# Performance work log

Hardware: AMD Instinct MI355X
Metric: run time of the kernel (lower is better)

The kernel has to match this reference:

```python
import jax, jax.numpy as jnp
import numpy as np

I_SIZE = 4096
H_SIZE = 2048
WIN = 10          # window_size
MAX_DEPTH = 6
EPS = 1e-9


def setup_inputs() -> dict:
    key = jax.random.key(0)
    ks = jax.random.split(key, 10)
    u = lambda k, s: jax.random.uniform(k, s, dtype=jnp.float32)
    n = lambda k, s: jax.random.normal(k, s, dtype=jnp.float32) * 0.02
    return {
        "input": u(ks[0], (WIN, I_SIZE)),
        "stack": u(ks[1], (1, H_SIZE, I_SIZE)),
        "stack_pointer": u(ks[2], (1, H_SIZE)),
        "input_pointer": u(ks[3], (1, WIN + 1)),
        "ff_w": n(ks[4], (I_SIZE, I_SIZE)), "ff_b": jnp.zeros((I_SIZE,), jnp.float32),
        "gate_w": n(ks[5], (2, 1)), "gate_b": jnp.zeros((2,), jnp.float32),
        "kin_w": n(ks[6], (I_SIZE, 2 * I_SIZE)), "kin_b": jnp.zeros((I_SIZE,), jnp.float32),
        "kouth_w": n(ks[7], (I_SIZE, I_SIZE)), "kouth_b": jnp.zeros((I_SIZE,), jnp.float32),
        "kouti_w": n(ks[8], (I_SIZE, I_SIZE)), "kouti_b": jnp.zeros((I_SIZE,), jnp.float32),
    }


def _forward(input, stack, stack_pointer, input_pointer,
             ff_w, ff_b, gate_w, gate_b, kin_w, kin_b,
             kouth_w, kouth_b, kouti_w, kouti_b):
    lsm = jax.nn.log_softmax
    lin = lambda x, w, b: jnp.matmul(x, w.T) + b

    def push(vec, stk, ptr):
        # stk: [1,H,I], ptr: [1,H], vec: [1,I] or [1,1,I]
        stk = stk * (1.0 - ptr)[..., None] + jnp.matmul(ptr[..., None], vec)
        ptr_new = jnp.concatenate([jnp.zeros((ptr.shape[0], 1), ptr.dtype), ptr[:, :-1]], axis=-1)
        return stk, ptr_new

    def pop(stk, ptr):
        ptr_new = jnp.concatenate([ptr[:, 1:], jnp.zeros((ptr.shape[0], 1), ptr.dtype)], axis=-1)
        s = jnp.sum(ptr_new, -1)                      # [1]
        norm = jnp.where(s > 0, ptr_new / jnp.where(s > 0, s, 1.0), ptr_new)
        outvec = jnp.matmul(norm, stk)                # [1,1,I]
        stk_new = (1.0 - ptr_new)[..., None] * stk
        ptr_new = ptr_new.at[:, 0].add(ptr[:, 0])
        return outvec, stk_new, ptr_new

    def get(inp, ptr):
        outvec = jnp.matmul(ptr[:, :-1], inp)         # [1,I]
        ptr_new = jnp.concatenate([jnp.zeros((ptr.shape[0], 1), ptr.dtype), ptr[:, :-1]], axis=-1)
        ptr_new = ptr_new.at[:, -1].add(ptr[:, -1])
        return outvec, ptr_new

    def kld(p, q):
        p = p + EPS
        q = q + EPS
        p = p / jnp.sum(p)
        q = q / jnp.sum(q)
        return jnp.sum(p * jnp.log(p / q))

    def calforward(invec, hvec):
        predvec = lsm(lin(hvec, ff_w, ff_b))
        perp_pred = kld(predvec, invec)
        inp_cat = jnp.concatenate([invec.reshape(1, 1, -1), hvec.reshape(1, 1, -1)], axis=-1)
        new_inp = jnp.exp(lsm(lin(inp_cat, kin_w, kin_b)))      # softmax, [1,1,I]
        proj_hvec = jnp.exp(lsm(lin(new_inp, kouth_w, kouth_b)))
        proj_invec = jnp.exp(lsm(lin(new_inp, kouti_w, kouti_b)))
        perp = perp_pred + kld(proj_invec, invec) / 2 + kld(proj_hvec, hvec) / 2
        gate = jnp.exp(lsm(lin(perp_pred.reshape(1), gate_w, gate_b)))  # [2]
        gate = jnp.where(jnp.sum(hvec) == 0, jnp.array([1.0, 0.0], gate.dtype),
                         jnp.where(jnp.sum(invec) == 0, jnp.array([0.0, 1.0], gate.dtype), gate))
        return gate, perp, new_inp

    stackmem, sptrmem, iptrmem, wldl, perps = [], [], [], [], []
    for ii in range(MAX_DEPTH):
        if ii == 0:
            invec, st1, sp1 = pop(stack, stack_pointer)
            hvec, st1, sp1 = pop(st1, sp1)
            gate, perp, new_inp = calforward(invec, hvec)
            st1, sp1 = push(new_inp, st1, sp1)
            stackmem.append(st1); sptrmem.append(sp1); iptrmem.append(input_pointer)
            wldl.append(gate[1]); perps.append(perp)
        else:
            ip2, st2, sp2 = input_pointer, stack, stack_pointer
            for _ in range(ii - 1):
                invec, ip2 = get(input, ip2)
                st2, sp2 = push(invec, st2, sp2)
            invec, ip2 = get(input, ip2)
            hvec, st2, sp2 = pop(st2, sp2)
            gate, perp, new_inp = calforward(invec, hvec)
            st2, sp2 = push(new_inp, st2, sp2)
            stackmem.append(st2); sptrmem.append(sp2); iptrmem.append(ip2)
            input_avail = 1.0 - ip2[0, -1]
            wldl.append((1.0 - wldl[ii - 1]) * gate[1] * input_avail)
            perps.append(perp)

    w = jnp.stack(wldl)
    w = w / jnp.sum(w)
    resperp = jnp.sum(w * jnp.stack(perps))
    new_stack = sum(w[i] * stackmem[i] for i in range(MAX_DEPTH))
    new_sp = sum(w[i] * sptrmem[i] for i in range(MAX_DEPTH))
    new_ip = sum(w[i] * iptrmem[i] for i in range(MAX_DEPTH))
    ssum = jnp.sum(new_sp, -1, keepdims=True)
    new_sp = jnp.where(ssum > 0, new_sp / jnp.where(ssum > 0, ssum, 1.0), new_sp)
    isum = jnp.sum(new_ip, -1, keepdims=True)
    new_ip = jnp.where(isum > 0, new_ip / jnp.where(isum > 0, isum, 1.0), new_ip)
    return resperp, new_stack, new_sp, new_ip


def reference(input, stack, stack_pointer, input_pointer,
              ff_w, ff_b, gate_w, gate_b, kin_w, kin_b,
              kouth_w, kouth_b, kouti_w, kouti_b):
    return _forward(input, stack, stack_pointer, input_pointer,
                    ff_w, ff_b, gate_w, gate_b, kin_w, kin_b,
                    kouth_w, kouth_b, kouti_w, kouti_b)
```

## Files before the change

kernel.cpp:

```cpp
#include <hip/hip_runtime.h>
#include <cfloat>
#include <cmath>

#define HH   2048
#define ISZ  4096
#define WN   10
#define ND   6
#define EPSF 1e-9f

#define O_WROW   0
#define O_GETW   14336
#define O_POPC   14464
#define O_AVAIL  14496
#define O_SCAL   14528
#define O_IPTR   14592
#define O_DFIN   14720
#define O_CNEW   27008
#define O_CFIN   39296
#define O_SPTR   88448
#define O_MW     100736
#define O_CEFF   104832
#define O_R      125312
#define O_NEWINP 153984
#define O_G      178560
#define O_HVEC   199040
#define O_IVEC   223616
#define O_YFF    248192
#define O_Z      272768
#define O_YH     297344
#define O_YI     321920

__device__ __forceinline__ float blockReduceSum(float v, float* sm){
  int ln = threadIdx.x & 63, w = threadIdx.x >> 6;
  #pragma unroll
  for (int o=32;o>0;o>>=1) v += __shfl_down(v,o);
  if (ln==0) sm[w]=v;
  __syncthreads();
  if (threadIdx.x==0){
    float r=0.f; int nw=(int)(blockDim.x>>6);
    for (int i=0;i<nw;i++) r+=sm[i];
    sm[16]=r;
  }
  __syncthreads();
  float r = sm[16];
  __syncthreads();
  return r;
}

__device__ __forceinline__ float blockReduceMax(float v, float* sm){
  int ln = threadIdx.x & 63, w = threadIdx.x >> 6;
  #pragma unroll
  for (int o=32;o>0;o>>=1) v = fmaxf(v,__shfl_down(v,o));
  if (ln==0) sm[w]=v;
  __syncthreads();
  if (threadIdx.x==0){
    float r=-FLT_MAX; int nw=(int)(blockDim.x>>6);
    for (int i=0;i<nw;i++) r=fmaxf(r,sm[i]);
    sm[16]=r;
  }
  __syncthreads();
  float r = sm[16];
  __syncthreads();
  return r;
}

__global__ __launch_bounds__(1024) void k_ptr_prep(
    const float* __restrict__ sp0g, const float* __restrict__ ip0g,
    float* __restrict__ ws)
{
  __shared__ float sp[HH], q[HH], D[HH];
  __shared__ float c[4][HH];
  __shared__ float red[17];
  const int d   = blockIdx.x;
  const int tid = threadIdx.x;

  float* Wrow = ws + O_WROW;
  float* getW = ws + O_GETW;
  float* popc = ws + O_POPC;
  float* Dfin = ws + O_DFIN;
  float* cnew = ws + O_CNEW;
  float* cfin = ws + O_CFIN;
  float* sptr = ws + O_SPTR;
  float* iptr = ws + O_IPTR;
  float* avail= ws + O_AVAIL;

  if (d==0 && tid==0){
    float ip[WN+1], nip[WN+1];
    for (int k=0;k<=WN;k++) ip[k]=ip0g[k];
    for (int k=0;k<=WN;k++) iptr[k]=ip[k];
    avail[0] = 1.f - ip[WN];
    for (int t=0;t<5;t++){
      for (int k=0;k<WN;k++) getW[t*16+k]=ip[k];
      nip[0]=0.f;
      for (int k=1;k<=WN;k++) nip[k]=ip[k-1];
      nip[WN] += ip[WN];
      for (int k=0;k<=WN;k++) ip[k]=nip[k];
      for (int k=0;k<=WN;k++) iptr[(t+1)*16+k]=ip[k];
      avail[t+1] = 1.f - ip[WN];
    }
  }

  #pragma unroll
  for (int jj=0;jj<2;jj++){ int j=tid+jj*1024; sp[j]=sp0g[j]; D[j]=1.f; }
  __syncthreads();

  if (d==0){
    #pragma unroll
    for (int jj=0;jj<2;jj++){ int j=tid+jj*1024; q[j]=(j<HH-1)? sp[j+1]:0.f; }
    float ls=0.f;
    #pragma unroll
    for (int jj=0;jj<2;jj++) ls += q[tid+jj*1024];
    float s = blockReduceSum(ls, red);
    float sc = (s>0.f)? 1.f/s : 1.f;
    #pragma unroll
    for (int jj=0;jj<2;jj++){
      int j=tid+jj*1024;
      float qq=q[j];
      Wrow[j] = qq*sc;
      D[j] = 1.f - qq;
      sp[j] = qq + ((j==0)? sp[0] : 0.f);
    }
    __syncthreads();
    #pragma unroll
    for (int jj=0;jj<2;jj++){ int j=tid+jj*1024; q[j]=(j<HH-1)? sp[j+1]:0.f; }
    ls=0.f;
    #pragma unroll
    for (int jj=0;jj<2;jj++) ls += q[tid+jj*1024];
    s = blockReduceSum(ls, red);
    sc = (s>0.f)? 1.f/s : 1.f;
    #pragma unroll
    for (int jj=0;jj<2;jj++){
      int j=tid+jj*1024;
      float qq=q[j];
      Wrow[HH+j] = qq*sc*D[j];
      D[j] *= (1.f-qq);
      sp[j] = qq + ((j==0)? sp[0] : 0.f);
    }
    __syncthreads();
    #pragma unroll
    for (int jj=0;jj<2;jj++){
      int j=tid+jj*1024;
      float p=sp[j];
      Dfin[j] = D[j]*(1.f-p);
      cnew[j] = p;
      sptr[j] = (j==0)? 0.f : sp[j-1];
    }
  } else {
    const int nterms = d-1;
    for (int t=0;t<nterms;t++){
      #pragma unroll
      for (int jj=0;jj<2;jj++){
        int j=tid+jj*1024;
        float p=sp[j], f=1.f-p;
        D[j]*=f;
        for (int u=0;u<t;u++) c[u][j]*=f;
        c[t][j]=p;
      }
      __syncthreads();
      float sv[2];
      #pragma unroll
      for (int jj=0;jj<2;jj++){ int j=tid+jj*1024; sv[jj]=(j==0)?0.f:sp[j-1]; }
      __syncthreads();
      #pragma unroll
      for (int jj=0;jj<2;jj++){ int j=tid+jj*1024; sp[j]=sv[jj]; }
      __syncthreads();
    }
    #pragma unroll
    for (int jj=0;jj<2;jj++){ int j=tid+jj*1024; q[j]=(j<HH-1)? sp[j+1]:0.f; }
    float ls=0.f;
    #pragma unroll
    for (int jj=0;jj<2;jj++) ls += q[tid+jj*1024];
    float s = blockReduceSum(ls, red);
    float sc = (s>0.f)? 1.f/s : 1.f;
    for (int t=0;t<nterms;t++){
      float pc=0.f;
      #pragma unroll
      for (int jj=0;jj<2;jj++){ int j=tid+jj*1024; pc += q[j]*sc*c[t][j]; }
      pc = blockReduceSum(pc, red);
      if (tid==0) popc[d*4+t]=pc;
    }
    #pragma unroll
    for (int jj=0;jj<2;jj++){
      int j=tid+jj*1024;
      float qq=q[j];
      Wrow[(1+d)*HH+j] = qq*sc*D[j];
      float f = 1.f-qq;
      D[j] *= f;
      for (int t=0;t<nterms;t++) c[t][j] *= f;
      sp[j] = qq + ((j==0)? sp[0] : 0.f);
    }
    __syncthreads();
    #pragma unroll
    for (int jj=0;jj<2;jj++){
      int j=tid+jj*1024;
      float p=sp[j], f=1.f-p;
      Dfin[d*HH+j] = D[j]*f;
      for (int t=0;t<nterms;t++) cfin[(d*4+t)*HH+j] = c[t][j]*f;
      cnew[d*HH+j] = p;
      sptr[d*HH+j] = (j==0)? 0.f : sp[j-1];
    }
  }
}

__global__ __launch_bounds__(256) void k_rowsum(
    const float* __restrict__ stk, const float* __restrict__ wrow,
    float* __restrict__ R)
{
  __shared__ float wsh[7][64];
  const int col = blockIdx.x*256 + threadIdx.x;
  const int r0  = blockIdx.y*64;
  for (int idx=threadIdx.x; idx<7*64; idx+=256){
    int k=idx>>6, r=idx&63;
    wsh[k][r]=wrow[k*HH + r0 + r];
  }
  __syncthreads();
  float a0=0,a1=0,a2=0,a3=0,a4=0,a5=0,a6=0;
  const float* sp = stk + (size_t)r0*ISZ + col;
  #pragma unroll 4
  for (int r=0;r<64;r++){
    float v = sp[(size_t)r*ISZ];
    a0+=wsh[0][r]*v; a1+=wsh[1][r]*v; a2+=wsh[2][r]*v; a3+=wsh[3][r]*v;
    a4+=wsh[4][r]*v; a5+=wsh[5][r]*v; a6+=wsh[6][r]*v;
  }
  atomicAdd(&R[0*ISZ+col],a0); atomicAdd(&R[1*ISZ+col],a1);
  atomicAdd(&R[2*ISZ+col],a2); atomicAdd(&R[3*ISZ+col],a3);
  atomicAdd(&R[4*ISZ+col],a4); atomicAdd(&R[5*ISZ+col],a5);
  atomicAdd(&R[6*ISZ+col],a6);
}

__global__ void k_gvec(const float* __restrict__ input,
                       const float* __restrict__ getW, float* __restrict__ g)
{
  int idx = blockIdx.x*256+threadIdx.x;
  if (idx >= 5*ISZ) return;
  int t = idx / ISZ, cx = idx % ISZ;
  float acc=0.f;
  #pragma unroll
  for (int k=0;k<WN;k++) acc += getW[t*16+k]*input[k*ISZ + cx];
  g[idx] = acc;
}

__global__ void k_build_hv(const float* __restrict__ R, const float* __restrict__ g,
                           const float* __restrict__ popc,
                           float* __restrict__ Hvec, float* __restrict__ Ivec)
{
  int idx = blockIdx.x*256+threadIdx.x;
  if (idx >= ND*ISZ) return;
  int d = idx/ISZ, cx = idx%ISZ;
  if (d==0){ Ivec[idx]=R[cx]; Hvec[idx]=R[ISZ+cx]; }
  else {
    Ivec[idx]=g[(d-1)*ISZ+cx];
    float h = R[(1+d)*ISZ+cx];
    for (int t=0;t<=d-2;t++) h += popc[d*4+t]*g[t*ISZ+cx];
    Hvec[idx]=h;
  }
}

__global__ __launch_bounds__(1024) void k_matvec6(
    const float* __restrict__ W, int ldw,
    const float* __restrict__ X, const float* __restrict__ bias,
    float* __restrict__ Y, int nrows, int accumulate)
{
  __shared__ float xs[6*ISZ];
  for (int idx=threadIdx.x; idx<6*ISZ; idx+=1024) xs[idx]=X[idx];
  __syncthreads();
  const int wv = threadIdx.x>>6, ln = threadIdx.x&63;
  const int row = blockIdx.x*16 + wv;
  if (row < nrows){
    const float* wr = W + (size_t)row*ldw;
    float a[6]={0,0,0,0,0,0};
    #pragma unroll 4
    for (int k=ln*4; k<ISZ; k+=256){
      float4 w4 = *(const float4*)(wr + k);
      #pragma unroll
      for (int d=0; d<6; d++){
        float4 x4 = *(const float4*)(xs + d*ISZ + k);
        a[d] += w4.x*x4.x + w4.y*x4.y + w4.z*x4.z + w4.w*x4.w;
      }
    }
    #pragma unroll
    for (int d=0;d<6;d++){
      float v = a[d];
      #pragma unroll
      for (int o=32;o>0;o>>=1) v += __shfl_down(v,o);
      if (ln==0){
        float r = v + (bias? bias[row] : 0.f);
        if (accumulate) Y[d*ISZ+row] += r;
        else            Y[d*ISZ+row]  = r;
      }
    }
  }
}

__global__ __launch_bounds__(1024) void k_s1(
    const float* __restrict__ yff, const float* __restrict__ zz,
    const float* __restrict__ Ivec, const float* __restrict__ Hvec,
    const float* __restrict__ gate_w, const float* __restrict__ gate_b,
    float* __restrict__ newinp, float* __restrict__ scal)
{
  __shared__ float sm[17];
  const int d = blockIdx.x, tid = threadIdx.x;
  const float* y  = yff + d*ISZ;
  const float* z  = zz  + d*ISZ;
  const float* iv = Ivec + d*ISZ;
  const float* hv = Hvec + d*ISZ;

  float m=-FLT_MAX;
  for (int cx=tid;cx<ISZ;cx+=1024) m=fmaxf(m,y[cx]);
  m = blockReduceMax(m,sm);
  float se=0.f;
  for (int cx=tid;cx<ISZ;cx+=1024) se += expf(y[cx]-m);
  se = blockReduceSum(se,sm);
  float lse = m + logf(se);

  float sP=0.f,sQ=0.f,sI=0.f,sH=0.f;
  for (int cx=tid;cx<ISZ;cx+=1024){
    sP += (y[cx]-lse)+EPSF;
    float ivv=iv[cx];
    sQ += ivv+EPSF; sI += ivv; sH += hv[cx];
  }
  sP=blockReduceSum(sP,sm); sQ=blockReduceSum(sQ,sm);
  sI=blockReduceSum(sI,sm); sH=blockReduceSum(sH,sm);

  float kk=0.f;
  for (int cx=tid;cx<ISZ;cx+=1024){
    float ph = ((y[cx]-lse)+EPSF)/sP;
    float qh = (iv[cx]+EPSF)/sQ;
    kk += ph*(logf(ph)-logf(qh));
  }
  kk = blockReduceSum(kk,sm);

  float m2=-FLT_MAX;
  for (int cx=tid;cx<ISZ;cx+=1024) m2=fmaxf(m2,z[cx]);
  m2=blockReduceMax(m2,sm);
  float se2=0.f;
  for (int cx=tid;cx<ISZ;cx+=1024) se2 += expf(z[cx]-m2);
  se2=blockReduceSum(se2,sm);
  float inv2=1.f/se2;
  for (int cx=tid;cx<ISZ;cx+=1024) newinp[d*ISZ+cx] = expf(z[cx]-m2)*inv2;

  if (tid==0){
    float pp=kk;
    float a0=gate_w[0]*pp+gate_b[0];
    float a1=gate_w[1]*pp+gate_b[1];
    float mg=fmaxf(a0,a1);
    float e0=expf(a0-mg), e1=expf(a1-mg);
    float g1=e1/(e0+e1);
    if (sH==0.f) g1=0.f;
    else if (sI==0.f) g1=1.f;
    scal[d]=pp; scal[6+d]=g1;
  }
}

__device__ float kld_softmax_vs(const float* __restrict__ lg,
                                const float* __restrict__ qv, float* sm)
{
  const int tid=threadIdx.x;
  float m=-FLT_MAX;
  for (int cx=tid;cx<ISZ;cx+=1024) m=fmaxf(m,lg[cx]);
  m=blockReduceMax(m,sm);
  float se=0.f;
  for (int cx=tid;cx<ISZ;cx+=1024) se+=expf(lg[cx]-m);
  se=blockReduceSum(se,sm);
  float inv=1.f/se;
  float sp=0.f,sq=0.f;
  for (int cx=tid;cx<ISZ;cx+=1024){ sp += expf(lg[cx]-m)*inv + EPSF; sq += qv[cx]+EPSF; }
  sp=blockReduceSum(sp,sm); sq=blockReduceSum(sq,sm);
  float kk=0.f;
  for (int cx=tid;cx<ISZ;cx+=1024){
    float ph=(expf(lg[cx]-m)*inv+EPSF)/sp;
    float qh=(qv[cx]+EPSF)/sq;
    kk += ph*(logf(ph)-logf(qh));
  }
  return blockReduceSum(kk,sm);
}

__global__ __launch_bounds__(1024) void k_s2(
    const float* __restrict__ yh, const float* __restrict__ yi,
    const float* __restrict__ Ivec, const float* __restrict__ Hvec,
    float* __restrict__ scal)
{
  __shared__ float sm[17];
  const int d=blockIdx.x;
  float kh = kld_softmax_vs(yh+d*ISZ, Hvec+d*ISZ, sm);
  float ki = kld_softmax_vs(yi+d*ISZ, Ivec+d*ISZ, sm);
  if (threadIdx.x==0) scal[12+d] = scal[d] + ki*0.5f + kh*0.5f;
}

__global__ void k_s3(float* __restrict__ ws, float* __restrict__ out){
  if (threadIdx.x==0 && blockIdx.x==0){
    const float* gate1 = ws + O_SCAL + 6;
    const float* perp  = ws + O_SCAL + 12;
    const float* avail = ws + O_AVAIL;
    float wl[ND];
    wl[0] = gate1[0];
    for (int i=1;i<ND;i++) wl[i] = (1.f - wl[i-1]) * gate1[i] * avail[i];
    float s=0.f; for (int i=0;i<ND;i++) s += wl[i];
    float rp=0.f;
    for (int i=0;i<ND;i++){ float wn = wl[i]/s; ws[O_SCAL+18+i]=wn; rp += wn*perp[i]; }
    out[0]=rp;
  }
}

__global__ __launch_bounds__(1024) void k_combine(float* __restrict__ ws,
                                                  float* __restrict__ out){
  __shared__ float sm[17];
  const int tid = threadIdx.x;
  float w[ND];
  #pragma unroll
  for (int d=0;d<ND;d++) w[d] = ws[O_SCAL+18+d];
  const float* Dfin = ws+O_DFIN; const float* cnew = ws+O_CNEW;
  const float* cfin = ws+O_CFIN; const float* sptr = ws+O_SPTR;
  float snl[2]; float mysum=0.f;
  for (int jj=0;jj<2;jj++){
    int j = tid + jj*1024;
    float mw=0.f, sn=0.f;
    float ce[10];
    #pragma unroll
    for (int d=0;d<ND;d++){
      mw += w[d]*Dfin[d*HH+j];
      sn += w[d]*sptr[d*HH+j];
      ce[d] = w[d]*cnew[d*HH+j];
    }
    #pragma unroll
    for (int t=0;t<4;t++){
      float a=0.f;
      for (int d=t+2;d<ND;d++) a += w[d]*cfin[(d*4+t)*HH+j];
      ce[6+t]=a;
    }
    ws[O_MW+j]=mw;
    #pragma unroll
    for (int v=0;v<10;v++) ws[O_CEFF + j*10 + v] = ce[v];
    snl[jj]=sn; mysum+=sn;
  }
  float ssum = blockReduceSum(mysum, sm);
  for (int jj=0;jj<2;jj++){
    int j = tid + jj*1024;
    out[1 + (size_t)HH*ISZ + j] = (ssum>0.f)? snl[jj]/ssum : snl[jj];
  }
  if (tid==0){
    const float* iptr = ws+O_IPTR;
    float ipn[WN+1]; float is=0.f;
    for (int k=0;k<=WN;k++){
      float a=0.f;
      for (int d=0;d<ND;d++) a += w[d]*iptr[d*16+k];
      ipn[k]=a; is+=a;
    }
    size_t base = 1 + (size_t)HH*ISZ + HH;
    for (int k=0;k<=WN;k++) out[base+k] = (is>0.f)? ipn[k]/is : ipn[k];
  }
}

__global__ __launch_bounds__(256) void k_stack_out(
    const float* __restrict__ stk, const float* __restrict__ V,
    const float* __restrict__ Mw, const float* __restrict__ Ceff,
    float* __restrict__ out)
{
  __shared__ float Vt[10*1024];
  const int c0 = blockIdx.x*1024;
  const int j0 = blockIdx.y*8;
  for (int idx=threadIdx.x; idx<10*1024; idx+=256){
    int v=idx>>10, cc=idx&1023;
    Vt[idx] = V[v*ISZ + c0 + cc];
  }
  __syncthreads();
  const int tx4 = threadIdx.x*4;
  for (int r=0;r<8;r++){
    int j=j0+r;
    float mw = Mw[j];
    float ce[10];
    #pragma unroll
    for (int v=0;v<10;v++) ce[v]=Ceff[j*10+v];
    float4 sv = *(const float4*)(stk + (size_t)j*ISZ + c0 + tx4);
    float o0 = mw*sv.x, o1 = mw*sv.y, o2 = mw*sv.z, o3 = mw*sv.w;
    #pragma unroll
    for (int v=0;v<10;v++){
      const float* vr = Vt + v*1024 + tx4;
      float cv=ce[v];
      o0 += cv*vr[0]; o1 += cv*vr[1]; o2 += cv*vr[2]; o3 += cv*vr[3];
    }
    float* op = out + 1 + (size_t)j*ISZ + c0 + tx4;
    op[0]=o0; op[1]=o1; op[2]=o2; op[3]=o3;
  }
}

extern "C" void kernel_launch(void* const* d_in, const int* in_sizes, int n_in,
                              void* d_out, int out_size, void* d_ws, size_t ws_size,
                              hipStream_t stream)
{
  (void)in_sizes; (void)n_in; (void)out_size; (void)ws_size;
  const float* input   = (const float*)d_in[0];
  const float* stack   = (const float*)d_in[1];
  const float* sp0     = (const float*)d_in[2];
  const float* ip0     = (const float*)d_in[3];
  const float* ff_w    = (const float*)d_in[4];
  const float* ff_b    = (const float*)d_in[5];
  const float* gate_w  = (const float*)d_in[6];
  const float* gate_b  = (const float*)d_in[7];
  const float* kin_w   = (const float*)d_in[8];
  const float* kin_b   = (const float*)d_in[9];
  const float* kouth_w = (const float*)d_in[10];
  const float* kouth_b = (const float*)d_in[11];
  const float* kouti_w = (const float*)d_in[12];
  const float* kouti_b = (const float*)d_in[13];
  float* out = (float*)d_out;
  float* ws  = (float*)d_ws;

  k_ptr_prep<<<ND,1024,0,stream>>>(sp0, ip0, ws);
  hipMemsetAsync(ws + O_R, 0, (size_t)7*ISZ*sizeof(float), stream);
  k_rowsum<<<dim3(16,32),256,0,stream>>>(stack, ws+O_WROW, ws+O_R);
  k_gvec<<<(5*ISZ+255)/256,256,0,stream>>>(input, ws+O_GETW, ws+O_G);
  k_build_hv<<<(ND*ISZ+255)/256,256,0,stream>>>(ws+O_R, ws+O_G, ws+O_POPC,
                                                ws+O_HVEC, ws+O_IVEC);
  k_matvec6<<<256,1024,0,stream>>>(kin_w,      8192, ws+O_IVEC, kin_b,   ws+O_Z,   ISZ, 0);
  k_matvec6<<<256,1024,0,stream>>>(ff_w,       4096, ws+O_HVEC, ff_b,    ws+O_YFF, ISZ, 0);
  k_matvec6<<<256,1024,0,stream>>>(kin_w+4096, 8192, ws+O_HVEC, nullptr, ws+O_Z,   ISZ, 1);
  k_s1<<<ND,1024,0,stream>>>(ws+O_YFF, ws+O_Z, ws+O_IVEC, ws+O_HVEC,
                             gate_w, gate_b, ws+O_NEWINP, ws+O_SCAL);
  k_matvec6<<<256,1024,0,stream>>>(kouth_w, 4096, ws+O_NEWINP, kouth_b, ws+O_YH, ISZ, 0);
  k_matvec6<<<256,1024,0,stream>>>(kouti_w, 4096, ws+O_NEWINP, kouti_b, ws+O_YI, ISZ, 0);
  k_s2<<<ND,1024,0,stream>>>(ws+O_YH, ws+O_YI, ws+O_IVEC, ws+O_HVEC, ws+O_SCAL);
  k_s3<<<1,64,0,stream>>>(ws, out);
  k_combine<<<1,1024,0,stream>>>(ws, out);
  k_stack_out<<<dim3(4,256),256,0,stream>>>(stack, ws+O_NEWINP, ws+O_MW, ws+O_CEFF, out);
}
```

Before: 209.5 us.

## Merge launches: batch matvecs, fuse vector build, single-pass reductions, drop atomics

The change cuts the pipeline from about fourteen launches to eight. The three first-stage matvecs become one 768-block grid and the two second-stage matvecs one 512-block grid, with the split z accumulation done in k_s1. The atomic rowsum with its memset is replaced by per-block partials reduced inside a new fused gvec/hv kernel. The softmax/KL stages keep their data in registers and use multi-value block reductions, and the combine weights are computed per block inside stack_out. This removes launch gaps and serial passes over memory, at the cost of redundant per-block weight computation and a small 32-block reduction kernel.

Measured after the change: 204.3 us. 1.03x faster.

```diff
diff --git a/kernel.cpp b/kernel.cpp
--- a/kernel.cpp
+++ b/kernel.cpp
@@ -18,17 +18,16 @@
 #define O_CNEW   27008
 #define O_CFIN   39296
 #define O_SPTR   88448
-#define O_MW     100736
-#define O_CEFF   104832
-#define O_R      125312
-#define O_NEWINP 153984
-#define O_G      178560
-#define O_HVEC   199040
-#define O_IVEC   223616
-#define O_YFF    248192
-#define O_Z      272768
-#define O_YH     297344
-#define O_YI     321920
+#define O_NEWINP 100736
+#define O_G      125312
+#define O_HVEC   145792
+#define O_IVEC   170368
+#define O_YFF    194944
+#define O_Z1     219520
+#define O_Z2     244096
+#define O_YH     268672
+#define O_YI     293248
+#define O_RPART  317824
 
 __device__ __forceinline__ float blockReduceSum(float v, float* sm){
   int ln = threadIdx.x & 63, w = threadIdx.x >> 6;
@@ -47,21 +46,40 @@
   return r;
 }
 
-__device__ __forceinline__ float blockReduceMax(float v, float* sm){
-  int ln = threadIdx.x & 63, w = threadIdx.x >> 6;
-  #pragma unroll
-  for (int o=32;o>0;o>>=1) v = fmaxf(v,__shfl_down(v,o));
-  if (ln==0) sm[w]=v;
+template<int N>
+__device__ __forceinline__ void bRedSumN(float* v, float* sm){
+  int ln=threadIdx.x&63, w=threadIdx.x>>6;
+  #pragma unroll
+  for (int o=32;o>0;o>>=1){
+    #pragma unroll
+    for (int i=0;i<N;i++) v[i]+=__shfl_down(v[i],o);
+  }
+  if (ln==0){ for (int i=0;i<N;i++) sm[w*N+i]=v[i]; }
   __syncthreads();
   if (threadIdx.x==0){
-    float r=-FLT_MAX; int nw=(int)(blockDim.x>>6);
-    for (int i=0;i<nw;i++) r=fmaxf(r,sm[i]);
-    sm[16]=r;
-  }
-  __syncthreads();
-  float r = sm[16];
-  __syncthreads();
-  return r;
+    for (int i=0;i<N;i++){ float r=0.f; for (int q=0;q<16;q++) r+=sm[q*N+i]; sm[16*N+i]=r; }
+  }
+  __syncthreads();
+  for (int i=0;i<N;i++) v[i]=sm[16*N+i];
+  __syncthreads();
+}
+
+template<int N>
+__device__ __forceinline__ void bRedMaxN(float* v, float* sm){
+  int ln=threadIdx.x&63, w=threadIdx.x>>6;
+  #pragma unroll
+  for (int o=32;o>0;o>>=1){
+    #pragma unroll
+    for (int i=0;i<N;i++) v[i]=fmaxf(v[i],__shfl_down(v[i],o));
+  }
+  if (ln==0){ for (int i=0;i<N;i++) sm[w*N+i]=v[i]; }
+  __syncthreads();
+  if (threadIdx.x==0){
+    for (int i=0;i<N;i++){ float r=-FLT_MAX; for (int q=0;q<16;q++) r=fmaxf(r,sm[q*N+i]); sm[16*N+i]=r; }
+  }
+  __syncthreads();
+  for (int i=0;i<N;i++) v[i]=sm[16*N+i];
+  __syncthreads();
 }
 
 __global__ __launch_bounds__(1024) void k_ptr_prep(
@@ -204,11 +222,12 @@
 
 __global__ __launch_bounds__(256) void k_rowsum(
     const float* __restrict__ stk, const float* __restrict__ wrow,
-    float* __restrict__ R)
+    float* __restrict__ Rp)
 {
   __shared__ float wsh[7][64];
   const int col = blockIdx.x*256 + threadIdx.x;
-  const int r0  = blockIdx.y*64;
+  const int by  = blockIdx.y;
+  const int r0  = by*64;
   for (int idx=threadIdx.x; idx<7*64; idx+=256){
     int k=idx>>6, r=idx&63;
     wsh[k][r]=wrow[k*HH + r0 + r];
@@ -222,228 +241,248 @@
     a0+=wsh[0][r]*v; a1+=wsh[1][r]*v; a2+=wsh[2][r]*v; a3+=wsh[3][r]*v;
     a4+=wsh[4][r]*v; a5+=wsh[5][r]*v; a6+=wsh[6][r]*v;
   }
-  atomicAdd(&R[0*ISZ+col],a0); atomicAdd(&R[1*ISZ+col],a1);
-  atomicAdd(&R[2*ISZ+col],a2); atomicAdd(&R[3*ISZ+col],a3);
-  atomicAdd(&R[4*ISZ+col],a4); atomicAdd(&R[5*ISZ+col],a5);
-  atomicAdd(&R[6*ISZ+col],a6);
-}
-
-__global__ void k_gvec(const float* __restrict__ input,
-                       const float* __restrict__ getW, float* __restrict__ g)
-{
-  int idx = blockIdx.x*256+threadIdx.x;
-  if (idx >= 5*ISZ) return;
-  int t = idx / ISZ, cx = idx % ISZ;
-  float acc=0.f;
-  #pragma unroll
-  for (int k=0;k<WN;k++) acc += getW[t*16+k]*input[k*ISZ + cx];
-  g[idx] = acc;
-}
-
-__global__ void k_build_hv(const float* __restrict__ R, const float* __restrict__ g,
-                           const float* __restrict__ popc,
-                           float* __restrict__ Hvec, float* __restrict__ Ivec)
-{
-  int idx = blockIdx.x*256+threadIdx.x;
-  if (idx >= ND*ISZ) return;
-  int d = idx/ISZ, cx = idx%ISZ;
-  if (d==0){ Ivec[idx]=R[cx]; Hvec[idx]=R[ISZ+cx]; }
-  else {
-    Ivec[idx]=g[(d-1)*ISZ+cx];
-    float h = R[(1+d)*ISZ+cx];
-    for (int t=0;t<=d-2;t++) h += popc[d*4+t]*g[t*ISZ+cx];
-    Hvec[idx]=h;
-  }
-}
-
-__global__ __launch_bounds__(1024) void k_matvec6(
+  Rp[(size_t)(by*7+0)*ISZ+col]=a0; Rp[(size_t)(by*7+1)*ISZ+col]=a1;
+  Rp[(size_t)(by*7+2)*ISZ+col]=a2; Rp[(size_t)(by*7+3)*ISZ+col]=a3;
+  Rp[(size_t)(by*7+4)*ISZ+col]=a4; Rp[(size_t)(by*7+5)*ISZ+col]=a5;
+  Rp[(size_t)(by*7+6)*ISZ+col]=a6;
+}
+
+__global__ __launch_bounds__(128) void k_hv(
+    const float* __restrict__ input, float* __restrict__ ws)
+{
+  __shared__ float gwS[80], pcS[24];
+  const int tid=threadIdx.x;
+  const int cx = blockIdx.x*128 + tid;
+  if (tid<80) gwS[tid]=ws[O_GETW+tid];
+  if (tid<24) pcS[tid]=ws[O_POPC+tid];
+  __syncthreads();
+  float inp[WN];
+  #pragma unroll
+  for (int k=0;k<WN;k++) inp[k]=input[k*ISZ+cx];
+  float g[5];
+  #pragma unroll
+  for (int t=0;t<5;t++){
+    float a=0.f;
+    #pragma unroll
+    for (int k=0;k<WN;k++) a += gwS[t*16+k]*inp[k];
+    g[t]=a;
+    ws[O_G + t*ISZ + cx]=a;
+  }
+  float R[7];
+  #pragma unroll
+  for (int k=0;k<7;k++){
+    float a=0.f;
+    for (int y=0;y<32;y++) a += ws[O_RPART + (size_t)(y*7+k)*ISZ + cx];
+    R[k]=a;
+  }
+  ws[O_IVEC + cx]=R[0];
+  ws[O_HVEC + cx]=R[1];
+  #pragma unroll
+  for (int d=1;d<ND;d++){
+    ws[O_IVEC + d*ISZ + cx] = g[d-1];
+    float h = R[1+d];
+    for (int t=0;t<=d-2;t++) h += pcS[d*4+t]*g[t];
+    ws[O_HVEC + d*ISZ + cx] = h;
+  }
+}
+
+__device__ __forceinline__ void mv_body(
     const float* __restrict__ W, int ldw,
-    const float* __restrict__ X, const float* __restrict__ bias,
-    float* __restrict__ Y, int nrows, int accumulate)
+    const float* __restrict__ Xg, const float* __restrict__ bias,
+    float* __restrict__ Y, int bb, float* xs)
+{
+  for (int idx=threadIdx.x; idx<6*ISZ; idx+=1024) xs[idx]=Xg[idx];
+  __syncthreads();
+  const int wv=threadIdx.x>>6, ln=threadIdx.x&63;
+  const int row = bb*16+wv;
+  const float* wr = W + (size_t)row*ldw;
+  float a[6]={0,0,0,0,0,0};
+  #pragma unroll 4
+  for (int k=ln*4; k<ISZ; k+=256){
+    float4 w4 = *(const float4*)(wr + k);
+    #pragma unroll
+    for (int d=0; d<6; d++){
+      float4 x4 = *(const float4*)(xs + d*ISZ + k);
+      a[d] += w4.x*x4.x + w4.y*x4.y + w4.z*x4.z + w4.w*x4.w;
+    }
+  }
+  #pragma unroll
+  for (int d=0;d<6;d++){
+    float v = a[d];
+    #pragma unroll
+    for (int o=32;o>0;o>>=1) v += __shfl_down(v,o);
+    if (ln==0) Y[d*ISZ+row] = v + (bias? bias[row] : 0.f);
+  }
+}
+
+__global__ __launch_bounds__(1024) void k_matvecA(
+    const float* __restrict__ ff_w, const float* __restrict__ ff_b,
+    const float* __restrict__ kin_w, const float* __restrict__ kin_b,
+    float* __restrict__ ws)
 {
   __shared__ float xs[6*ISZ];
-  for (int idx=threadIdx.x; idx<6*ISZ; idx+=1024) xs[idx]=X[idx];
-  __syncthreads();
-  const int wv = threadIdx.x>>6, ln = threadIdx.x&63;
-  const int row = blockIdx.x*16 + wv;
-  if (row < nrows){
-    const float* wr = W + (size_t)row*ldw;
-    float a[6]={0,0,0,0,0,0};
-    #pragma unroll 4
-    for (int k=ln*4; k<ISZ; k+=256){
-      float4 w4 = *(const float4*)(wr + k);
-      #pragma unroll
-      for (int d=0; d<6; d++){
-        float4 x4 = *(const float4*)(xs + d*ISZ + k);
-        a[d] += w4.x*x4.x + w4.y*x4.y + w4.z*x4.z + w4.w*x4.w;
-      }
-    }
-    #pragma unroll
-    for (int d=0;d<6;d++){
-      float v = a[d];
-      #pragma unroll
-      for (int o=32;o>0;o>>=1) v += __shfl_down(v,o);
-      if (ln==0){
-        float r = v + (bias? bias[row] : 0.f);
-        if (accumulate) Y[d*ISZ+row] += r;
-        else            Y[d*ISZ+row]  = r;
-      }
-    }
-  }
+  const int task = blockIdx.x >> 8, bb = blockIdx.x & 255;
+  if (task==0)      mv_body(kin_w,     2*ISZ, ws+O_IVEC, kin_b,   ws+O_Z1,  bb, xs);
+  else if (task==1) mv_body(ff_w,      ISZ,   ws+O_HVEC, ff_b,    ws+O_YFF, bb, xs);
+  else              mv_body(kin_w+ISZ, 2*ISZ, ws+O_HVEC, nullptr, ws+O_Z2,  bb, xs);
+}
+
+__global__ __launch_bounds__(1024) void k_matvecB(
+    const float* __restrict__ kouth_w, const float* __restrict__ kouth_b,
+    const float* __restrict__ kouti_w, const float* __restrict__ kouti_b,
+    float* __restrict__ ws)
+{
+  __shared__ float xs[6*ISZ];
+  const int task = blockIdx.x >> 8, bb = blockIdx.x & 255;
+  if (task==0) mv_body(kouth_w, ISZ, ws+O_NEWINP, kouth_b, ws+O_YH, bb, xs);
+  else         mv_body(kouti_w, ISZ, ws+O_NEWINP, kouti_b, ws+O_YI, bb, xs);
 }
 
 __global__ __launch_bounds__(1024) void k_s1(
-    const float* __restrict__ yff, const float* __restrict__ zz,
-    const float* __restrict__ Ivec, const float* __restrict__ Hvec,
     const float* __restrict__ gate_w, const float* __restrict__ gate_b,
-    float* __restrict__ newinp, float* __restrict__ scal)
-{
-  __shared__ float sm[17];
-  const int d = blockIdx.x, tid = threadIdx.x;
-  const float* y  = yff + d*ISZ;
-  const float* z  = zz  + d*ISZ;
-  const float* iv = Ivec + d*ISZ;
-  const float* hv = Hvec + d*ISZ;
-
-  float m=-FLT_MAX;
-  for (int cx=tid;cx<ISZ;cx+=1024) m=fmaxf(m,y[cx]);
-  m = blockReduceMax(m,sm);
-  float se=0.f;
-  for (int cx=tid;cx<ISZ;cx+=1024) se += expf(y[cx]-m);
-  se = blockReduceSum(se,sm);
-  float lse = m + logf(se);
-
-  float sP=0.f,sQ=0.f,sI=0.f,sH=0.f;
-  for (int cx=tid;cx<ISZ;cx+=1024){
-    sP += (y[cx]-lse)+EPSF;
-    float ivv=iv[cx];
-    sQ += ivv+EPSF; sI += ivv; sH += hv[cx];
-  }
-  sP=blockReduceSum(sP,sm); sQ=blockReduceSum(sQ,sm);
-  sI=blockReduceSum(sI,sm); sH=blockReduceSum(sH,sm);
-
-  float kk=0.f;
-  for (int cx=tid;cx<ISZ;cx+=1024){
-    float ph = ((y[cx]-lse)+EPSF)/sP;
-    float qh = (iv[cx]+EPSF)/sQ;
-    kk += ph*(logf(ph)-logf(qh));
-  }
-  kk = blockReduceSum(kk,sm);
-
-  float m2=-FLT_MAX;
-  for (int cx=tid;cx<ISZ;cx+=1024) m2=fmaxf(m2,z[cx]);
-  m2=blockReduceMax(m2,sm);
-  float se2=0.f;
-  for (int cx=tid;cx<ISZ;cx+=1024) se2 += expf(z[cx]-m2);
-  se2=blockReduceSum(se2,sm);
-  float inv2=1.f/se2;
-  for (int cx=tid;cx<ISZ;cx+=1024) newinp[d*ISZ+cx] = expf(z[cx]-m2)*inv2;
+    float* __restrict__ ws)
+{
+  __shared__ float sm[96];
+  const int d=blockIdx.x, tid=threadIdx.x;
+  const float* y  = ws+O_YFF + d*ISZ;
+  const float* z1 = ws+O_Z1  + d*ISZ;
+  const float* z2 = ws+O_Z2  + d*ISZ;
+  const float* iv = ws+O_IVEC+ d*ISZ;
+  const float* hv = ws+O_HVEC+ d*ISZ;
+
+  float yv[4], zv[4], ivv[4], hvv[4];
+  #pragma unroll
+  for (int i=0;i<4;i++){
+    int cx=tid+i*1024;
+    yv[i]=y[cx]; zv[i]=z1[cx]+z2[cx]; ivv[i]=iv[cx]; hvv[i]=hv[cx];
+  }
+  float mx[2]={-FLT_MAX,-FLT_MAX};
+  #pragma unroll
+  for (int i=0;i<4;i++){ mx[0]=fmaxf(mx[0],yv[i]); mx[1]=fmaxf(mx[1],zv[i]); }
+  bRedMaxN<2>(mx,sm);
+
+  float s5[5]={0,0,0,0,0};
+  #pragma unroll
+  for (int i=0;i<4;i++){
+    s5[0]+=expf(yv[i]-mx[0]); s5[1]+=expf(zv[i]-mx[1]);
+    s5[2]+=yv[i]; s5[3]+=ivv[i]; s5[4]+=hvv[i];
+  }
+  bRedSumN<5>(s5,sm);
+  const float lse = mx[0]+logf(s5[0]);
+  const float sP  = s5[2] - (float)ISZ*lse + (float)ISZ*EPSF;
+  const float sQ  = s5[3] + (float)ISZ*EPSF;
+  const float inv2= 1.f/s5[1];
+
+  float kk[1]={0.f};
+  #pragma unroll
+  for (int i=0;i<4;i++){
+    int cx=tid+i*1024;
+    ws[O_NEWINP + d*ISZ + cx] = expf(zv[i]-mx[1])*inv2;
+    float ph=((yv[i]-lse)+EPSF)/sP;
+    float qh=(ivv[i]+EPSF)/sQ;
+    kk[0]+=ph*(logf(ph)-logf(qh));
+  }
+  bRedSumN<1>(kk,sm);
 
   if (tid==0){
-    float pp=kk;
+    float pp=kk[0];
     float a0=gate_w[0]*pp+gate_b[0];
     float a1=gate_w[1]*pp+gate_b[1];
     float mg=fmaxf(a0,a1);
     float e0=expf(a0-mg), e1=expf(a1-mg);
     float g1=e1/(e0+e1);
-    if (sH==0.f) g1=0.f;
-    else if (sI==0.f) g1=1.f;
-    scal[d]=pp; scal[6+d]=g1;
-  }
-}
-
-__device__ float kld_softmax_vs(const float* __restrict__ lg,
-                                const float* __restrict__ qv, float* sm)
-{
+    if (s5[4]==0.f) g1=0.f;
+    else if (s5[3]==0.f) g1=1.f;
+    ws[O_SCAL+d]=pp; ws[O_SCAL+6+d]=g1;
+    ws[O_SCAL+24+d]=sQ;
+    ws[O_SCAL+30+d]=s5[4]+(float)ISZ*EPSF;
+  }
+}
+
+__global__ __launch_bounds__(1024) void k_s2(float* __restrict__ ws)
+{
+  __shared__ float sm[96];
+  const int d=blockIdx.x, tid=threadIdx.x;
+  const float* yh = ws+O_YH  + d*ISZ;
+  const float* yi = ws+O_YI  + d*ISZ;
+  const float* hv = ws+O_HVEC+ d*ISZ;
+  const float* iv = ws+O_IVEC+ d*ISZ;
+
+  float yhv[4], yiv[4], hvv[4], ivv[4];
+  #pragma unroll
+  for (int i=0;i<4;i++){
+    int cx=tid+i*1024;
+    yhv[i]=yh[cx]; yiv[i]=yi[cx]; hvv[i]=hv[cx]; ivv[i]=iv[cx];
+  }
+  float mx[2]={-FLT_MAX,-FLT_MAX};
+  #pragma unroll
+  for (int i=0;i<4;i++){ mx[0]=fmaxf(mx[0],yhv[i]); mx[1]=fmaxf(mx[1],yiv[i]); }
+  bRedMaxN<2>(mx,sm);
+  float se[2]={0,0};
+  #pragma unroll
+  for (int i=0;i<4;i++){ se[0]+=expf(yhv[i]-mx[0]); se[1]+=expf(yiv[i]-mx[1]); }
+  bRedSumN<2>(se,sm);
+  const float invh=1.f/se[0], invi=1.f/se[1];
+  const float spc = 1.f + (float)ISZ*EPSF;
+  const float sqh = ws[O_SCAL+30+d], sqi = ws[O_SCAL+24+d];
+
+  float kk[2]={0,0};
+  #pragma unroll
+  for (int i=0;i<4;i++){
+    float ph=(expf(yhv[i]-mx[0])*invh+EPSF)/spc;
+    float qh=(hvv[i]+EPSF)/sqh;
+    kk[0]+=ph*(logf(ph)-logf(qh));
+    float pi=(expf(yiv[i]-mx[1])*invi+EPSF)/spc;
+    float qi=(ivv[i]+EPSF)/sqi;
+    kk[1]+=pi*(logf(pi)-logf(qi));
+  }
+  bRedSumN<2>(kk,sm);
+  if (tid==0) ws[O_SCAL+12+d] = ws[O_SCAL+d] + 0.5f*(kk[0]+kk[1]);
+}
+
+__global__ __launch_bounds__(1024) void k_fin(float* __restrict__ ws,
+                                              float* __restrict__ out)
+{
+  __shared__ float sm[32];
+  __shared__ float wsh[ND];
   const int tid=threadIdx.x;
-  float m=-FLT_MAX;
-  for (int cx=tid;cx<ISZ;cx+=1024) m=fmaxf(m,lg[cx]);
-  m=blockReduceMax(m,sm);
-  float se=0.f;
-  for (int cx=tid;cx<ISZ;cx+=1024) se+=expf(lg[cx]-m);
-  se=blockReduceSum(se,sm);
-  float inv=1.f/se;
-  float sp=0.f,sq=0.f;
-  for (int cx=tid;cx<ISZ;cx+=1024){ sp += expf(lg[cx]-m)*inv + EPSF; sq += qv[cx]+EPSF; }
-  sp=blockReduceSum(sp,sm); sq=blockReduceSum(sq,sm);
-  float kk=0.f;
-  for (int cx=tid;cx<ISZ;cx+=1024){
-    float ph=(expf(lg[cx]-m)*inv+EPSF)/sp;
-    float qh=(qv[cx]+EPSF)/sq;
-    kk += ph*(logf(ph)-logf(qh));
-  }
-  return blockReduceSum(kk,sm);
-}
-
-__global__ __launch_bounds__(1024) void k_s2(
-    const float* __restrict__ yh, const float* __restrict__ yi,
-    const float* __restrict__ Ivec, const float* __restrict__ Hvec,
-    float* __restrict__ scal)
-{
-  __shared__ float sm[17];
-  const int d=blockIdx.x;
-  float kh = kld_softmax_vs(yh+d*ISZ, Hvec+d*ISZ, sm);
-  float ki = kld_softmax_vs(yi+d*ISZ, Ivec+d*ISZ, sm);
-  if (threadIdx.x==0) scal[12+d] = scal[d] + ki*0.5f + kh*0.5f;
-}
-
-__global__ void k_s3(float* __restrict__ ws, float* __restrict__ out){
-  if (threadIdx.x==0 && blockIdx.x==0){
-    const float* gate1 = ws + O_SCAL + 6;
-    const float* perp  = ws + O_SCAL + 12;
-    const float* avail = ws + O_AVAIL;
-    float wl[ND];
-    wl[0] = gate1[0];
-    for (int i=1;i<ND;i++) wl[i] = (1.f - wl[i-1]) * gate1[i] * avail[i];
-    float s=0.f; for (int i=0;i<ND;i++) s += wl[i];
+  if (tid==0){
+    const float* g1=ws+O_SCAL+6; const float* pp=ws+O_SCAL+12; const float* av=ws+O_AVAIL;
+    float wl[ND]; wl[0]=g1[0];
+    for (int i=1;i<ND;i++) wl[i]=(1.f-wl[i-1])*g1[i]*av[i];
+    float s=0.f; for (int i=0;i<ND;i++) s+=wl[i];
     float rp=0.f;
-    for (int i=0;i<ND;i++){ float wn = wl[i]/s; ws[O_SCAL+18+i]=wn; rp += wn*perp[i]; }
+    for (int i=0;i<ND;i++){ float wn=wl[i]/s; wsh[i]=wn; rp+=wn*pp[i]; }
     out[0]=rp;
   }
-}
-
-__global__ __launch_bounds__(1024) void k_combine(float* __restrict__ ws,
-                                                  float* __restrict__ out){
-  __shared__ float sm[17];
-  const int tid = threadIdx.x;
+  __syncthreads();
   float w[ND];
   #pragma unroll
-  for (int d=0;d<ND;d++) w[d] = ws[O_SCAL+18+d];
-  const float* Dfin = ws+O_DFIN; const float* cnew = ws+O_CNEW;
-  const float* cfin = ws+O_CFIN; const float* sptr = ws+O_SPTR;
-  float snl[2]; float mysum=0.f;
+  for (int dd=0;dd<ND;dd++) w[dd]=wsh[dd];
+  const float* sptr=ws+O_SPTR;
+  float snl[2], ms=0.f;
+  #pragma unroll
   for (int jj=0;jj<2;jj++){
-    int j = tid + jj*1024;
-    float mw=0.f, sn=0.f;
-    float ce[10];
-    #pragma unroll
-    for (int d=0;d<ND;d++){
-      mw += w[d]*Dfin[d*HH+j];
-      sn += w[d]*sptr[d*HH+j];
-      ce[d] = w[d]*cnew[d*HH+j];
-    }
-    #pragma unroll
-    for (int t=0;t<4;t++){
-      float a=0.f;
-      for (int d=t+2;d<ND;d++) a += w[d]*cfin[(d*4+t)*HH+j];
-      ce[6+t]=a;
-    }
-    ws[O_MW+j]=mw;
-    #pragma unroll
-    for (int v=0;v<10;v++) ws[O_CEFF + j*10 + v] = ce[v];
-    snl[jj]=sn; mysum+=sn;
-  }
-  float ssum = blockReduceSum(mysum, sm);
+    int j=tid+jj*1024;
+    float sn=0.f;
+    #pragma unroll
+    for (int dd=0;dd<ND;dd++) sn += w[dd]*sptr[dd*HH+j];
+    snl[jj]=sn; ms+=sn;
+  }
+  float t[1]={ms};
+  bRedSumN<1>(t,sm);
+  float ssum=t[0];
+  #pragma unroll
   for (int jj=0;jj<2;jj++){
-    int j = tid + jj*1024;
+    int j=tid+jj*1024;
     out[1 + (size_t)HH*ISZ + j] = (ssum>0.f)? snl[jj]/ssum : snl[jj];
   }
   if (tid==0){
-    const float* iptr = ws+O_IPTR;
+    const float* iptr=ws+O_IPTR;
     float ipn[WN+1]; float is=0.f;
     for (int k=0;k<=WN;k++){
       float a=0.f;
-      for (int d=0;d<ND;d++) a += w[d]*iptr[d*16+k];
+      for (int dd=0;dd<ND;dd++) a += w[dd]*iptr[dd*16+k];
       ipn[k]=a; is+=a;
     }
     size_t base = 1 + (size_t)HH*ISZ + HH;
@@ -452,31 +491,57 @@
 }
 
 __global__ __launch_bounds__(256) void k_stack_out(
-    const float* __restrict__ stk, const float* __restrict__ V,
-    const float* __restrict__ Mw, const float* __restrict__ Ceff,
+    const float* __restrict__ stk, const float* __restrict__ ws,
     float* __restrict__ out)
 {
   __shared__ float Vt[10*1024];
+  __shared__ float wsh[ND];
+  __shared__ float mwS[8];
+  __shared__ float ceS[8][10];
+  const int tid=threadIdx.x;
   const int c0 = blockIdx.x*1024;
   const int j0 = blockIdx.y*8;
-  for (int idx=threadIdx.x; idx<10*1024; idx+=256){
+
+  if (tid==0){
+    const float* g1=ws+O_SCAL+6; const float* av=ws+O_AVAIL;
+    float wl[ND]; wl[0]=g1[0];
+    for (int i=1;i<ND;i++) wl[i]=(1.f-wl[i-1])*g1[i]*av[i];
+    float s=0.f; for (int i=0;i<ND;i++) s+=wl[i];
+    for (int i=0;i<ND;i++) wsh[i]=wl[i]/s;
+  }
+  const float* V = ws+O_NEWINP;
+  for (int idx=tid; idx<10*1024; idx+=256){
     int v=idx>>10, cc=idx&1023;
     Vt[idx] = V[v*ISZ + c0 + cc];
   }
   __syncthreads();
-  const int tx4 = threadIdx.x*4;
+  if (tid<8){
+    int j=j0+tid;
+    float mw=0.f, ce[10]={0,0,0,0,0,0,0,0,0,0};
+    for (int dd=0;dd<ND;dd++){
+      float wd=wsh[dd];
+      mw    += wd*ws[O_DFIN+dd*HH+j];
+      ce[dd] = wd*ws[O_CNEW+dd*HH+j];
+    }
+    for (int t=0;t<4;t++){
+      float a=0.f;
+      for (int dd=t+2;dd<ND;dd++) a += wsh[dd]*ws[O_CFIN+(dd*4+t)*HH+j];
+      ce[6+t]=a;
+    }
+    mwS[tid]=mw;
+    for (int v=0;v<10;v++) ceS[tid][v]=ce[v];
+  }
+  __syncthreads();
+  const int tx4 = tid*4;
   for (int r=0;r<8;r++){
     int j=j0+r;
-    float mw = Mw[j];
-    float ce[10];
-    #pragma unroll
-    for (int v=0;v<10;v++) ce[v]=Ceff[j*10+v];
+    float mw = mwS[r];
     float4 sv = *(const float4*)(stk + (size_t)j*ISZ + c0 + tx4);
     float o0 = mw*sv.x, o1 = mw*sv.y, o2 = mw*sv.z, o3 = mw*sv.w;
     #pragma unroll
     for (int v=0;v<10;v++){
       const float* vr = Vt + v*1024 + tx4;
-      float cv=ce[v];
+      float cv=ceS[r][v];
       o0 += cv*vr[0]; o1 += cv*vr[1]; o2 += cv*vr[2]; o3 += cv*vr[3];
     }
     float* op = out + 1 + (size_t)j*ISZ + c0 + tx4;
@@ -507,20 +572,12 @@
   float* ws  = (float*)d_ws;
 
   k_ptr_prep<<<ND,1024,0,stream>>>(sp0, ip0, ws);
-  hipMemsetAsync(ws + O_R, 0, (size_t)7*ISZ*sizeof(float), stream);
-  k_rowsum<<<dim3(16,32),256,0,stream>>>(stack, ws+O_WROW, ws+O_R);
-  k_gvec<<<(5*ISZ+255)/256,256,0,stream>>>(input, ws+O_GETW, ws+O_G);
-  k_build_hv<<<(ND*ISZ+255)/256,256,0,stream>>>(ws+O_R, ws+O_G, ws+O_POPC,
-                                                ws+O_HVEC, ws+O_IVEC);
-  k_matvec6<<<256,1024,0,stream>>>(kin_w,      8192, ws+O_IVEC, kin_b,   ws+O_Z,   ISZ, 0);
-  k_matvec6<<<256,1024,0,stream>>>(ff_w,       4096, ws+O_HVEC, ff_b,    ws+O_YFF, ISZ, 0);
-  k_matvec6<<<256,1024,0,stream>>>(kin_w+4096, 8192, ws+O_HVEC, nullptr, ws+O_Z,   ISZ, 1);
-  k_s1<<<ND,1024,0,stream>>>(ws+O_YFF, ws+O_Z, ws+O_IVEC, ws+O_HVEC,
-                             gate_w, gate_b, ws+O_NEWINP, ws+O_SCAL);
-  k_matvec6<<<256,1024,0,stream>>>(kouth_w, 4096, ws+O_NEWINP, kouth_b, ws+O_YH, ISZ, 0);
-  k_matvec6<<<256,1024,0,stream>>>(kouti_w, 4096, ws+O_NEWINP, kouti_b, ws+O_YI, ISZ, 0);
-  k_s2<<<ND,1024,0,stream>>>(ws+O_YH, ws+O_YI, ws+O_IVEC, ws+O_HVEC, ws+O_SCAL);
-  k_s3<<<1,64,0,stream>>>(ws, out);
-  k_combine<<<1,1024,0,stream>>>(ws, out);
-  k_stack_out<<<dim3(4,256),256,0,stream>>>(stack, ws+O_NEWINP, ws+O_MW, ws+O_CEFF, out);
-}
+  k_rowsum<<<dim3(16,32),256,0,stream>>>(stack, ws+O_WROW, ws+O_RPART);
+  k_hv<<<32,128,0,stream>>>(input, ws);
+  k_matvecA<<<768,1024,0,stream>>>(ff_w, ff_b, kin_w, kin_b, ws);
+  k_s1<<<ND,1024,0,stream>>>(gate_w, gate_b, ws);
+  k_matvecB<<<512,1024,0,stream>>>(kouth_w, kouth_b, kouti_w, kouti_b, ws);
+  k_s2<<<ND,1024,0,stream>>>(ws);
+  k_stack_out<<<dim3(4,256),256,0,stream>>>(stack, ws, out);
+  k_fin<<<1,1024,0,stream>>>(ws, out);
+}
```
